# Kernel tuning notes

Hardware: AMD Instinct MI355X
Metric: run time of the kernel (lower is better)

The kernel has to match this reference:

```python
import jax, jax.numpy as jnp
import numpy as np

N_HEADS = 16
B, T, H, HA = 4, 8192, 1024, 1024

def _split_heads(x, n_heads):
    n, t, d = x.shape
    return x.reshape(n, t, n_heads, d // n_heads).transpose(0, 2, 1, 3)  # [n,h,t,dh]

def setup_inputs() -> dict:
    key = jax.random.key(0)
    ks = jax.random.split(key, 9)
    s = 0.02
    return {
        "q": jax.random.normal(ks[0], (B, T, H), jnp.float32),
        "k": jax.random.normal(ks[1], (B, T, H), jnp.float32),
        "v": jax.random.normal(ks[2], (B, T, H), jnp.float32),
        "mask_q": jnp.ones((B, T), jnp.float32),
        "mask_attn": jnp.ones((B, T), jnp.float32),
        "Wq": jax.random.normal(ks[3], (HA, H), jnp.float32) * s,
        "bq": jnp.zeros((HA,), jnp.float32),
        "Wk": jax.random.normal(ks[4], (HA, H), jnp.float32) * s,
        "bk": jnp.zeros((HA,), jnp.float32),
        "Wv": jax.random.normal(ks[5], (H, H), jnp.float32) * s,
        "bv": jnp.zeros((H,), jnp.float32),
    }

def reference(q, k, v, mask_q, mask_attn, Wq, bq, Wk, bk, Wv, bv):
    # projections (dropout = identity in eval)
    qp = q @ Wq.T + bq
    kp = k @ Wk.T + bk
    vp = v @ Wv.T + bv
    qh = _split_heads(qp, N_HEADS)  # [n,h,t,dqk]
    kh = _split_heads(kp, N_HEADS)
    vh = _split_heads(vp, N_HEADS)  # [n,h,t,dv]
    # additive masking (efficient_attn, outer_attn != 'scaled' branch)
    kh = kh - 10000.0 * (1.0 - mask_attn)[:, None, :, None]
    qh = qh - 10000.0 * (1.0 - mask_q)[:, None, :, None]
    dv = vh.shape[-1]  # d // n_heads where d = hidden (from v)
    # softmax over sequence dim of k, then k^T @ v : [n,h,dqk,dv]
    ctx = jnp.einsum('nhtd,nhte->nhde', jax.nn.softmax(kh, axis=2), vh)
    ctx = ctx / jnp.sqrt(jnp.float32(dv))
    # softmax over feature dim of q, then q @ ctx : [n,h,t,dv]
    out = jnp.einsum('nhtd,nhde->nhte', jax.nn.softmax(qh, axis=-1), ctx)
    n, h, t, e = out.shape
    return out.transpose(0, 2, 1, 3).reshape(n, t, h * e)
```

## Files before the change

### kernel.cpp

```cpp
#include <hip/hip_runtime.h>
#include <hip/hip_bf16.h>
#include <math.h>

#define B_  4
#define T_  8192
#define H_  1024
#define NHEAD 16
#define DH  64
#define BT  (B_*T_)

typedef __attribute__((ext_vector_type(8))) short bf16x8;
typedef __attribute__((ext_vector_type(4))) float f32x4;
typedef __attribute__((ext_vector_type(2))) float f32x2;
typedef __attribute__((ext_vector_type(2))) unsigned short u16x2;
typedef __attribute__((ext_vector_type(4))) unsigned short u16x4;
typedef __attribute__((ext_vector_type(8))) unsigned short u16x8;

static __device__ __forceinline__ float bf2f(unsigned short u) {
  union { unsigned int i; float f; } x; x.i = ((unsigned int)u) << 16; return x.f;
}
static __device__ __forceinline__ unsigned short f2bf(float f) {
  union { float f; unsigned int i; } x; x.f = f;
  unsigned int r = x.i + 0x7fffu + ((x.i >> 16) & 1u);
  return (unsigned short)(r >> 16);
}

#define GL2LDS(gptr, sptr) \
  __builtin_amdgcn_global_load_lds((const __attribute__((address_space(1))) void*)(gptr), \
                                   (__attribute__((address_space(3))) void*)(sptr), 16, 0, 0)

__global__ void cvt_kernel(const float* __restrict__ in, unsigned short* __restrict__ out, int n4) {
  int i = blockIdx.x * blockDim.x + threadIdx.x;
  int stride = gridDim.x * blockDim.x;
  for (int idx = i; idx < n4; idx += stride) {
    float4 v = reinterpret_cast<const float4*>(in)[idx];
    u16x4 o;
    o.x = f2bf(v.x); o.y = f2bf(v.y); o.z = f2bf(v.z); o.w = f2bf(v.w);
    reinterpret_cast<u16x4*>(out)[idx] = o;
  }
}

__global__ __launch_bounds__(256, 2) void gemm_nt(
    const unsigned short* __restrict__ A,
    const unsigned short* __restrict__ Bm,
    const float* __restrict__ bias,
    unsigned short* __restrict__ C) {
  const int K = 1024, N = 1024;
  __shared__ unsigned short sA[128 * 32];
  __shared__ unsigned short sB[128 * 32];
  const int tid  = threadIdx.x;
  const int lane = tid & 63;
  const int wid  = tid >> 6;
  const int orig = blockIdx.y * 8 + blockIdx.x;
  const int swz  = (orig & 7) * 256 + (orig >> 3);
  const int bm = (swz >> 3) * 128, bn = (swz & 7) * 128;
  const int wm = (wid >> 1) * 64,  wn = (wid & 1) * 64;

  f32x4 acc[4][4];
#pragma unroll
  for (int nn = 0; nn < 4; ++nn) {
    float bv = bias[bn + wn + nn * 16 + (lane & 15)];
    f32x4 sp = {bv, bv, bv, bv};
#pragma unroll
    for (int mm = 0; mm < 4; ++mm) acc[mm][nn] = sp;
  }

  const int srow = tid >> 2;
  const int scol = (tid & 3) * 8;
  const unsigned short* gA0 = A  + (size_t)(bm + srow) * K + scol;
  const unsigned short* gA1 = gA0 + (size_t)64 * K;
  const unsigned short* gB0 = Bm + (size_t)(bn + srow) * K + scol;
  const unsigned short* gB1 = gB0 + (size_t)64 * K;
  char* dA = (char*)&sA[0] + wid * 1024;
  char* dB = (char*)&sB[0] + wid * 1024;

  const char* fA = (const char*)&sA[0] + (wm + (lane & 15)) * 64 + (lane >> 4) * 16;
  const char* fB = (const char*)&sB[0] + (wn + (lane & 15)) * 64 + (lane >> 4) * 16;

  for (int k0 = 0; k0 < K; k0 += 32) {
    GL2LDS(gA0 + k0, dA);
    GL2LDS(gA1 + k0, dA + 4096);
    GL2LDS(gB0 + k0, dB);
    GL2LDS(gB1 + k0, dB + 4096);
    __syncthreads();
    bf16x8 av[4], bv_[4];
#pragma unroll
    for (int mm = 0; mm < 4; ++mm) av[mm]  = *(const bf16x8*)(fA + mm * 1024);
#pragma unroll
    for (int nn = 0; nn < 4; ++nn) bv_[nn] = *(const bf16x8*)(fB + nn * 1024);
#pragma unroll
    for (int mm = 0; mm < 4; ++mm)
#pragma unroll
      for (int nn = 0; nn < 4; ++nn)
        acc[mm][nn] = __builtin_amdgcn_mfma_f32_16x16x32_bf16(av[mm], bv_[nn], acc[mm][nn], 0, 0, 0);
    __syncthreads();
  }

  const int crow = bm + wm + (lane >> 4) * 4;
  const int ccol = bn + wn + (lane & 15);
#pragma unroll
  for (int mm = 0; mm < 4; ++mm)
#pragma unroll
    for (int j = 0; j < 4; ++j) {
      unsigned short* cp = C + (size_t)(crow + mm * 16 + j) * N + ccol;
#pragma unroll
      for (int nn = 0; nn < 4; ++nn) cp[nn * 16] = f2bf(acc[mm][nn][j]);
    }
}

__global__ __launch_bounds__(256, 2) void phase1(
    const unsigned short* __restrict__ Pk,
    const unsigned short* __restrict__ Pv,
    const float* __restrict__ mask_attn,
    float* __restrict__ Upart,
    float* __restrict__ cspart) {
  const int chunk = blockIdx.x;
  const int nh = blockIdx.y;
  const int n = nh >> 4, h = nh & 15;
  const int tid = threadIdx.x, lane = tid & 63, wid = tid >> 6;
  __shared__ __align__(16) unsigned short ekT[64 * 256];
  __shared__ __align__(16) unsigned short vpT[64 * 256];

  f32x4 acc[5];
#pragma unroll
  for (int i = 0; i < 5; ++i) acc[i] = (f32x4){0.f, 0.f, 0.f, 0.f};
  bf16x8 ones;
#pragma unroll
  for (int j = 0; j < 8; ++j) ones[j] = (short)0x3f80;

  const int isV = tid >> 7;
  const int slot0 = tid & 127;
  const unsigned short* src = isV ? Pv : Pk;
  unsigned short* dstT = isV ? vpT : ekT;

  const int arow = wid * 16 + (lane & 15);
  const int aswz = ((arow & 7) ^ ((arow >> 3) & 7)) << 4;

  for (int stage = 0; stage < 4; ++stage) {
    if (stage) __syncthreads();
#pragma unroll
    for (int r = 0; r < 2; ++r) {
      const int slot = slot0 + r * 128;
      const int toct = slot >> 3;
      const int d0   = (slot & 7) * 8;
      const int tbase = chunk * 1024 + stage * 256 + toct * 8;
      u16x8 in[8];
#pragma unroll
      for (int s = 0; s < 8; ++s)
        in[s] = *(const u16x8*)(src + (size_t)(n * T_ + tbase + s) * H_ + h * DH + d0);
      if (!isV) {
#pragma unroll
        for (int s = 0; s < 8; ++s) {
          const float madd = -10000.f * (1.f - mask_attn[n * T_ + tbase + s]);
          u16x8 o;
#pragma unroll
          for (int j = 0; j < 8; ++j) o[j] = f2bf(__expf(bf2f(in[s][j]) + madd));
          in[s] = o;
        }
      }
#pragma unroll
      for (int i = 0; i < 8; ++i) {
        u16x8 o;
#pragma unroll
        for (int s = 0; s < 8; ++s) o[s] = in[s][i];
        const int d = d0 + i;
        const int boff = (toct * 16) ^ (((d & 7) ^ ((d >> 3) & 7)) << 4);
        *(u16x8*)((char*)dstT + d * 512 + boff) = o;
      }
    }
    __syncthreads();
#pragma unroll
    for (int kk = 0; kk < 8; ++kk) {
      const int koff = kk * 64 + (lane >> 4) * 16;
      bf16x8 af = *(const bf16x8*)((const char*)ekT + arow * 512 + (koff ^ aswz));
      acc[4] = __builtin_amdgcn_mfma_f32_16x16x32_bf16(af, ones, acc[4], 0, 0, 0);
#pragma unroll
      for (int nn = 0; nn < 4; ++nn) {
        const int brow = nn * 16 + (lane & 15);
        const int bswz = ((brow & 7) ^ ((brow >> 3) & 7)) << 4;
        bf16x8 bf_ = *(const bf16x8*)((const char*)vpT + brow * 512 + (koff ^ bswz));
        acc[nn] = __builtin_amdgcn_mfma_f32_16x16x32_bf16(af, bf_, acc[nn], 0, 0, 0);
      }
    }
  }

  const int d = wid * 16 + (lane >> 4) * 4;
  const int e = lane & 15;
  float* up = Upart + ((size_t)(chunk * 64 + nh) * 64) * 64;
#pragma unroll
  for (int nn = 0; nn < 4; ++nn)
#pragma unroll
    for (int j = 0; j < 4; ++j)
      up[(size_t)(d + j) * 64 + nn * 16 + e] = acc[nn][j];
  if (e == 0)
#pragma unroll
    for (int j = 0; j < 4; ++j)
      cspart[((size_t)chunk * 64 + nh) * 64 + d + j] = acc[4][j];
}

__global__ void ctxbuild(const float* __restrict__ Upart,
                         const float* __restrict__ cspart,
                         unsigned short* __restrict__ ctxT) {
  const int nh = blockIdx.x, tid = threadIdx.x;
  __shared__ float cs[64];
  if (tid < 64) {
    float s = 0;
    for (int c = 0; c < 8; ++c) s += cspart[((size_t)c * 64 + nh) * 64 + tid];
    cs[tid] = s;
  }
  __syncthreads();
  const int d0 = (tid >> 4) * 4, e0 = (tid & 15) * 4;
#pragma unroll
  for (int i = 0; i < 4; ++i) {
    const float inv = 0.125f / cs[d0 + i];
#pragma unroll
    for (int j = 0; j < 4; ++j) {
      float s = 0;
      for (int c = 0; c < 8; ++c)
        s += Upart[((size_t)(c * 64 + nh) * 64 + d0 + i) * 64 + e0 + j];
      ctxT[((size_t)nh * 64 + (e0 + j)) * 64 + (d0 + i)] = f2bf(s * inv);
    }
  }
}

__global__ __launch_bounds__(256) void outk(
    const unsigned short* __restrict__ Pq,
    const unsigned short* __restrict__ ctxT,
    float* __restrict__ Out) {
  const int tb = blockIdx.x;
  const int nh = blockIdx.y;
  const int n = nh >> 4, h = nh & 15;
  const int tid = threadIdx.x, lane = tid & 63, wid = tid >> 6;
  __shared__ unsigned short sp[128][72];

  bf16x8 breg[2][4];
#pragma unroll
  for (int ks = 0; ks < 2; ++ks)
#pragma unroll
    for (int nn = 0; nn < 4; ++nn)
      breg[ks][nn] = *(const bf16x8*)(ctxT + ((size_t)nh * 64 + nn * 16 + (lane & 15)) * 64
                                      + ks * 32 + (lane >> 4) * 8);

  const int r = tid >> 1, half = tid & 1;
  const int t0 = tb * 128;
  const size_t qoff = (size_t)(n * T_ + t0 + r) * H_ + h * DH + half * 32;
  u16x8 qv[4];
#pragma unroll
  for (int s = 0; s < 4; ++s) qv[s] = *(const u16x8*)(Pq + qoff + s * 8);
  float e[32]; float sum = 0.f;
#pragma unroll
  for (int s = 0; s < 4; ++s)
#pragma unroll
    for (int j = 0; j < 8; ++j) { float x = __expf(bf2f(qv[s][j])); e[s * 8 + j] = x; sum += x; }
  sum += __shfl_xor(sum, 1);
  const float inv = 1.f / sum;
#pragma unroll
  for (int s = 0; s < 4; ++s) {
    u16x8 pb;
#pragma unroll
    for (int j = 0; j < 8; ++j) pb[j] = f2bf(e[s * 8 + j] * inv);
    *(u16x8*)&sp[r][half * 32 + s * 8] = pb;
  }
  __syncthreads();

  f32x4 acc[2][4];
  f32x4 z = {0.f, 0.f, 0.f, 0.f};
#pragma unroll
  for (int mm = 0; mm < 2; ++mm)
#pragma unroll
    for (int nn = 0; nn < 4; ++nn) acc[mm][nn] = z;
  const int wm = wid * 32;
#pragma unroll
  for (int ks = 0; ks < 2; ++ks) {
    bf16x8 av[2];
#pragma unroll
    for (int mm = 0; mm < 2; ++mm)
      av[mm] = *(const bf16x8*)((const char*)&sp[0][0]
               + (wm + mm * 16 + (lane & 15)) * 144 + ks * 64 + (lane >> 4) * 16);
#pragma unroll
    for (int mm = 0; mm < 2; ++mm)
#pragma unroll
      for (int nn = 0; nn < 4; ++nn)
        acc[mm][nn] = __builtin_amdgcn_mfma_f32_16x16x32_bf16(av[mm], breg[ks][nn], acc[mm][nn], 0, 0, 0);
  }

#pragma unroll
  for (int mm = 0; mm < 2; ++mm)
#pragma unroll
    for (int j = 0; j < 4; ++j) {
      const int row = t0 + wm + mm * 16 + (lane >> 4) * 4 + j;
      float* op = Out + ((size_t)n * T_ + row) * H_ + h * DH + (lane & 15);
#pragma unroll
      for (int nn = 0; nn < 4; ++nn) op[nn * 16] = acc[mm][nn][j];
    }
}

extern "C" void kernel_launch(void* const* d_in, const int* in_sizes, int n_in,
                              void* d_out, int out_size, void* d_ws, size_t ws_size,
                              hipStream_t stream) {
  const float* q  = (const float*)d_in[0];
  const float* k  = (const float*)d_in[1];
  const float* v  = (const float*)d_in[2];
  const float* mask_attn = (const float*)d_in[4];
  const float* Wq = (const float*)d_in[5];
  const float* bq = (const float*)d_in[6];
  const float* Wk = (const float*)d_in[7];
  const float* bk = (const float*)d_in[8];
  const float* Wv = (const float*)d_in[9];
  const float* bv = (const float*)d_in[10];
  float* out = (float*)d_out;

  char* ws = (char*)d_ws;
  size_t off = 0;
  unsigned short* Xb = (unsigned short*)(ws + off); off += (size_t)BT * H_ * 2;
  unsigned short* Wb = (unsigned short*)(ws + off); off += (size_t)3 * H_ * H_ * 2;
  unsigned short* Pq = (unsigned short*)(ws + off); off += (size_t)BT * H_ * 2;
  unsigned short* Pk = (unsigned short*)(ws + off); off += (size_t)BT * H_ * 2;
  unsigned short* Pv = (unsigned short*)(ws + off); off += (size_t)BT * H_ * 2;
  float* Upart  = (float*)(ws + off); off += (size_t)8 * 64 * 64 * 64 * 4;
  float* cspart = (float*)(ws + off); off += (size_t)8 * 64 * 64 * 4;
  unsigned short* ctxT = (unsigned short*)(ws + off); off += (size_t)64 * 64 * 64 * 2;

  dim3 blk(256);
  const int nW4 = H_ * H_ / 4;
  cvt_kernel<<<dim3(512), blk, 0, stream>>>(Wq, Wb + 0 * H_ * H_, nW4);
  cvt_kernel<<<dim3(512), blk, 0, stream>>>(Wk, Wb + 1 * H_ * H_, nW4);
  cvt_kernel<<<dim3(512), blk, 0, stream>>>(Wv, Wb + 2 * H_ * H_, nW4);

  const int nX4 = BT * H_ / 4;
  dim3 ggrid(8, 256);
  cvt_kernel<<<dim3(2048), blk, 0, stream>>>(k, Xb, nX4);
  gemm_nt<<<ggrid, blk, 0, stream>>>(Xb, Wb + 1 * H_ * H_, bk, Pk);
  cvt_kernel<<<dim3(2048), blk, 0, stream>>>(v, Xb, nX4);
  gemm_nt<<<ggrid, blk, 0, stream>>>(Xb, Wb + 2 * H_ * H_, bv, Pv);
  cvt_kernel<<<dim3(2048), blk, 0, stream>>>(q, Xb, nX4);
  gemm_nt<<<ggrid, blk, 0, stream>>>(Xb, Wb + 0 * H_ * H_, bq, Pq);

  phase1<<<dim3(8, 64), blk, 0, stream>>>(Pk, Pv, mask_attn, Upart, cspart);
  ctxbuild<<<dim3(64), blk, 0, stream>>>(Upart, cspart, ctxT);
  outk<<<dim3(64, 64), blk, 0, stream>>>(Pq, ctxT, out);
}
```

Before: 447.0 us.

## Replace projection GEMM with 256x256 double-buffered pipelined MFMA kernel

Rewrites the bf16 projection GEMM to use 256x256 block tiles with 8 waves, a 64-wide K step and two LDS buffers filled by direct global-to-LDS loads. A swizzled LDS layout reduces bank conflicts, and prefetching of the next tiles is interleaved with MFMA quadrants using raw barriers, manual vmcnt waits and priority hints. The aim is to raise arithmetic intensity and hide global-load latency that the old single-buffered 128x128 kernel exposed. It uses 128KB of LDS per block, which limits occupancy, and depends on hand-counted waitcnt correctness.

```diff
diff --git a/kernel.cpp b/kernel.cpp
--- a/kernel.cpp
+++ b/kernel.cpp
@@ -28,6 +28,9 @@
 #define GL2LDS(gptr, sptr) \
   __builtin_amdgcn_global_load_lds((const __attribute__((address_space(1))) void*)(gptr), \
                                    (__attribute__((address_space(3))) void*)(sptr), 16, 0, 0)
+
+#define BAR() do { asm volatile("" ::: "memory"); __builtin_amdgcn_s_barrier(); \
+                   asm volatile("" ::: "memory"); } while (0)
 
 __global__ void cvt_kernel(const float* __restrict__ in, unsigned short* __restrict__ out, int n4) {
   int i = blockIdx.x * blockDim.x + threadIdx.x;
@@ -40,71 +43,122 @@
   }
 }
 
-__global__ __launch_bounds__(256, 2) void gemm_nt(
+__global__ __launch_bounds__(512, 2) void gemm256(
     const unsigned short* __restrict__ A,
     const unsigned short* __restrict__ Bm,
     const float* __restrict__ bias,
     unsigned short* __restrict__ C) {
   const int K = 1024, N = 1024;
-  __shared__ unsigned short sA[128 * 32];
-  __shared__ unsigned short sB[128 * 32];
-  const int tid  = threadIdx.x;
-  const int lane = tid & 63;
-  const int wid  = tid >> 6;
-  const int orig = blockIdx.y * 8 + blockIdx.x;
-  const int swz  = (orig & 7) * 256 + (orig >> 3);
-  const int bm = (swz >> 3) * 128, bn = (swz & 7) * 128;
-  const int wm = (wid >> 1) * 64,  wn = (wid & 1) * 64;
-
-  f32x4 acc[4][4];
-#pragma unroll
-  for (int nn = 0; nn < 4; ++nn) {
-    float bv = bias[bn + wn + nn * 16 + (lane & 15)];
+  __shared__ char lds[131072];
+  const int tid = threadIdx.x, lane = tid & 63, wid = tid >> 6;
+  const int orig = blockIdx.x;
+  const int swzb = (orig & 7) * 64 + (orig >> 3);
+  const int bm = (swzb >> 2) * 256, bn = (swzb & 3) * 256;
+  const int wm = wid >> 2, wn = wid & 3;
+
+  const int sr   = wid * 8 + (lane >> 3);
+  const int scol = ((lane & 7) * 8) ^ ((lane & 32) >> 1);
+  const unsigned short* gA = A  + (size_t)(bm + sr) * K + scol;
+  const unsigned short* gB = Bm + (size_t)(bn + sr) * K + scol;
+  const int dstw = wid * 1024;
+
+  const int aflag = (lane & 4) ? 32 : 0;
+  const int lcol  = ((lane >> 4) * 16) ^ aflag;
+  const int aoff0 = (wm * 128 + (lane & 15)) * 128 + lcol;
+  const int boff0 = 32768 + (wn * 64 + (lane & 15)) * 128 + lcol;
+
+  f32x4 acc[8][4];
+#pragma unroll
+  for (int fn = 0; fn < 4; ++fn) {
+    float bv = bias[bn + wn * 64 + fn * 16 + (lane & 15)];
     f32x4 sp = {bv, bv, bv, bv};
 #pragma unroll
-    for (int mm = 0; mm < 4; ++mm) acc[mm][nn] = sp;
-  }
-
-  const int srow = tid >> 2;
-  const int scol = (tid & 3) * 8;
-  const unsigned short* gA0 = A  + (size_t)(bm + srow) * K + scol;
-  const unsigned short* gA1 = gA0 + (size_t)64 * K;
-  const unsigned short* gB0 = Bm + (size_t)(bn + srow) * K + scol;
-  const unsigned short* gB1 = gB0 + (size_t)64 * K;
-  char* dA = (char*)&sA[0] + wid * 1024;
-  char* dB = (char*)&sB[0] + wid * 1024;
-
-  const char* fA = (const char*)&sA[0] + (wm + (lane & 15)) * 64 + (lane >> 4) * 16;
-  const char* fB = (const char*)&sB[0] + (wn + (lane & 15)) * 64 + (lane >> 4) * 16;
-
-  for (int k0 = 0; k0 < K; k0 += 32) {
-    GL2LDS(gA0 + k0, dA);
-    GL2LDS(gA1 + k0, dA + 4096);
-    GL2LDS(gB0 + k0, dB);
-    GL2LDS(gB1 + k0, dB + 4096);
-    __syncthreads();
-    bf16x8 av[4], bv_[4];
-#pragma unroll
-    for (int mm = 0; mm < 4; ++mm) av[mm]  = *(const bf16x8*)(fA + mm * 1024);
-#pragma unroll
-    for (int nn = 0; nn < 4; ++nn) bv_[nn] = *(const bf16x8*)(fB + nn * 1024);
-#pragma unroll
-    for (int mm = 0; mm < 4; ++mm)
-#pragma unroll
-      for (int nn = 0; nn < 4; ++nn)
-        acc[mm][nn] = __builtin_amdgcn_mfma_f32_16x16x32_bf16(av[mm], bv_[nn], acc[mm][nn], 0, 0, 0);
-    __syncthreads();
-  }
-
-  const int crow = bm + wm + (lane >> 4) * 4;
-  const int ccol = bn + wn + (lane & 15);
-#pragma unroll
-  for (int mm = 0; mm < 4; ++mm)
+    for (int fm = 0; fm < 8; ++fm) acc[fm][fn] = sp;
+  }
+
+  bf16x8 aF[4][2], bF[4][2];
+
+  auto stA4 = [&](int buf, int kt) {
+    char* d = lds + buf * 65536 + dstw;
+    const unsigned short* g = gA + kt * 64;
+    GL2LDS(g, d);
+    GL2LDS(g + (size_t)64  * K, d + 8192);
+    GL2LDS(g + (size_t)128 * K, d + 16384);
+    GL2LDS(g + (size_t)192 * K, d + 24576);
+  };
+  auto stB = [&](int buf, int kt) {
+    char* d = lds + buf * 65536 + 32768 + dstw;
+    const unsigned short* g = gB + kt * 64;
+    GL2LDS(g, d);
+    GL2LDS(g + (size_t)64  * K, d + 8192);
+    GL2LDS(g + (size_t)128 * K, d + 16384);
+    GL2LDS(g + (size_t)192 * K, d + 24576);
+  };
+  auto loadA = [&](int buf, int mh) {
+#pragma unroll
+    for (int f = 0; f < 4; ++f)
+#pragma unroll
+      for (int ks = 0; ks < 2; ++ks)
+        aF[f][ks] = *(const bf16x8*)(lds + buf * 65536 + aoff0 + (mh * 4 + f) * 2048 + ks * 64);
+  };
+  auto loadB = [&](int buf, int nh) {
+#pragma unroll
+    for (int f = 0; f < 2; ++f)
+#pragma unroll
+      for (int ks = 0; ks < 2; ++ks)
+        bF[nh * 2 + f][ks] = *(const bf16x8*)(lds + buf * 65536 + boff0 + (nh * 2 + f) * 2048 + ks * 64);
+  };
+  auto quad = [&](int mh, int nh) {
+    __builtin_amdgcn_s_setprio(1);
+#pragma unroll
+    for (int f = 0; f < 4; ++f)
+#pragma unroll
+      for (int g2 = 0; g2 < 2; ++g2)
+#pragma unroll
+        for (int ks = 0; ks < 2; ++ks)
+          acc[mh * 4 + f][nh * 2 + g2] = __builtin_amdgcn_mfma_f32_16x16x32_bf16(
+              aF[f][ks], bF[nh * 2 + g2][ks], acc[mh * 4 + f][nh * 2 + g2], 0, 0, 0);
+    __builtin_amdgcn_s_setprio(0);
+  };
+
+  stA4(0, 0); stB(0, 0);
+  stA4(1, 1); stB(1, 1);
+  asm volatile("s_waitcnt vmcnt(8)" ::: "memory");
+  BAR();
+
+#define KTILE(t, STG, WSTR, DOW)                              \
+  {                                                           \
+    const int b_ = (t) & 1;                                   \
+    loadA(b_, 0); loadB(b_, 0);                               \
+    quad(0, 0);                                               \
+    BAR();                                                    \
+    loadB(b_, 1);                                             \
+    quad(0, 1);                                               \
+    BAR();                                                    \
+    if (STG) stB(b_, (t) + 2);                                \
+    loadA(b_, 1);                                             \
+    quad(1, 0);                                               \
+    BAR();                                                    \
+    if (STG) stA4(b_, (t) + 2);                               \
+    quad(1, 1);                                               \
+    if (DOW) { asm volatile("s_waitcnt vmcnt(" WSTR ")" ::: "memory"); } \
+    BAR();                                                    \
+  }
+
+  for (int t = 0; t < 14; ++t) KTILE(t, 1, "8", 1)
+  KTILE(14, 0, "0", 1)
+  KTILE(15, 0, "0", 0)
+#undef KTILE
+
+  const int crow0 = bm + wm * 128 + (lane >> 4) * 4;
+  const int ccol0 = bn + wn * 64 + (lane & 15);
+#pragma unroll
+  for (int fm = 0; fm < 8; ++fm)
 #pragma unroll
     for (int j = 0; j < 4; ++j) {
-      unsigned short* cp = C + (size_t)(crow + mm * 16 + j) * N + ccol;
-#pragma unroll
-      for (int nn = 0; nn < 4; ++nn) cp[nn * 16] = f2bf(acc[mm][nn][j]);
+      unsigned short* cp = C + (size_t)(crow0 + fm * 16 + j) * N + ccol0;
+#pragma unroll
+      for (int fn = 0; fn < 4; ++fn) cp[fn * 16] = f2bf(acc[fm][fn][j]);
     }
 }
 
@@ -328,13 +382,14 @@
   cvt_kernel<<<dim3(512), blk, 0, stream>>>(Wv, Wb + 2 * H_ * H_, nW4);
 
   const int nX4 = BT * H_ / 4;
-  dim3 ggrid(8, 256);
+  dim3 gblk(512);
+  dim3 ggrid(512);
   cvt_kernel<<<dim3(2048), blk, 0, stream>>>(k, Xb, nX4);
-  gemm_nt<<<ggrid, blk, 0, stream>>>(Xb, Wb + 1 * H_ * H_, bk, Pk);
+  gemm256<<<ggrid, gblk, 0, stream>>>(Xb, Wb + 1 * H_ * H_, bk, Pk);
   cvt_kernel<<<dim3(2048), blk, 0, stream>>>(v, Xb, nX4);
-  gemm_nt<<<ggrid, blk, 0, stream>>>(Xb, Wb + 2 * H_ * H_, bv, Pv);
+  gemm256<<<ggrid, gblk, 0, stream>>>(Xb, Wb + 2 * H_ * H_, bv, Pv);
   cvt_kernel<<<dim3(2048), blk, 0, stream>>>(q, Xb, nX4);
-  gemm_nt<<<ggrid, blk, 0, stream>>>(Xb, Wb + 0 * H_ * H_, bq, Pq);
+  gemm256<<<ggrid, gblk, 0, stream>>>(Xb, Wb + 0 * H_ * H_, bq, Pq);
 
   phase1<<<dim3(8, 64), blk, 0, stream>>>(Pk, Pv, mask_attn, Upart, cspart);
   ctxbuild<<<dim3(64), blk, 0, stream>>>(Upart, cspart, ctxT);
```

Measured after the change: 417.8 us. 6.5% less time.

## Fuse fp32-to-bf16 input conversion into double-buffered pipelined projection GEMM

Applied to the files above, without the earlier changes.

The separate activation conversion kernels are removed, and the projection GEMM now reads fp32 inputs directly. It converts them to bf16 in registers and writes them into swizzled LDS. The K loop is restructured into a double-buffered, software-pipelined schedule with manual waitcnt and barriers, plus s_setprio around the MFMAs. This removes three full read/write passes over the activations and aims to overlap global loads with MFMA. In exchange the GEMM reads the A operand from global memory at twice the bytes, and the hand-tuned waitcnt sequence is fragile.

```diff
diff --git a/kernel.cpp b/kernel.cpp
--- a/kernel.cpp
+++ b/kernel.cpp
@@ -28,6 +28,9 @@
 #define GL2LDS(gptr, sptr) \
   __builtin_amdgcn_global_load_lds((const __attribute__((address_space(1))) void*)(gptr), \
                                    (__attribute__((address_space(3))) void*)(sptr), 16, 0, 0)
+
+#define BAR() do { asm volatile("" ::: "memory"); __builtin_amdgcn_s_barrier(); \
+                   asm volatile("" ::: "memory"); } while (0)
 
 __global__ void cvt_kernel(const float* __restrict__ in, unsigned short* __restrict__ out, int n4) {
   int i = blockIdx.x * blockDim.x + threadIdx.x;
@@ -40,21 +43,32 @@
   }
 }
 
-__global__ __launch_bounds__(256, 2) void gemm_nt(
-    const unsigned short* __restrict__ A,
+__global__ __launch_bounds__(256, 3) void gemm128f(
+    const float* __restrict__ A,
     const unsigned short* __restrict__ Bm,
     const float* __restrict__ bias,
     unsigned short* __restrict__ C) {
   const int K = 1024, N = 1024;
-  __shared__ unsigned short sA[128 * 32];
-  __shared__ unsigned short sB[128 * 32];
-  const int tid  = threadIdx.x;
-  const int lane = tid & 63;
-  const int wid  = tid >> 6;
+  __shared__ char lds[32768];
+  const int tid = threadIdx.x, lane = tid & 63, wid = tid >> 6;
   const int orig = blockIdx.y * 8 + blockIdx.x;
   const int swz  = (orig & 7) * 256 + (orig >> 3);
   const int bm = (swz >> 3) * 128, bn = (swz & 7) * 128;
-  const int wm = (wid >> 1) * 64,  wn = (wid & 1) * 64;
+  const int wm = (wid >> 1) * 64, wn = (wid & 1) * 64;
+
+  const int r_  = tid >> 1;
+  const int ch  = (tid & 1) * 16;
+  const float* gA32 = A + (size_t)(bm + r_) * K + ch;
+  const int awbase = r_ * 64;
+  const int awswz  = ((r_ >> 1) & 3) << 4;
+
+  const int sr2  = wid * 16 + (lane >> 2);
+  const int scol = ((lane & 3) * 8) ^ (((lane >> 3) & 3) << 3);
+  const unsigned short* gB = Bm + (size_t)(bn + sr2) * K + scol;
+  const int dstw = wid * 1024;
+
+  const int fswz = (((lane & 15) >> 1) & 3) << 4;
+  const int kc   = ((lane >> 4) * 16) ^ fswz;
 
   f32x4 acc[4][4];
 #pragma unroll
@@ -65,36 +79,84 @@
     for (int mm = 0; mm < 4; ++mm) acc[mm][nn] = sp;
   }
 
-  const int srow = tid >> 2;
-  const int scol = (tid & 3) * 8;
-  const unsigned short* gA0 = A  + (size_t)(bm + srow) * K + scol;
-  const unsigned short* gA1 = gA0 + (size_t)64 * K;
-  const unsigned short* gB0 = Bm + (size_t)(bn + srow) * K + scol;
-  const unsigned short* gB1 = gB0 + (size_t)64 * K;
-  char* dA = (char*)&sA[0] + wid * 1024;
-  char* dB = (char*)&sB[0] + wid * 1024;
-
-  const char* fA = (const char*)&sA[0] + (wm + (lane & 15)) * 64 + (lane >> 4) * 16;
-  const char* fB = (const char*)&sB[0] + (wn + (lane & 15)) * 64 + (lane >> 4) * 16;
-
-  for (int k0 = 0; k0 < K; k0 += 32) {
-    GL2LDS(gA0 + k0, dA);
-    GL2LDS(gA1 + k0, dA + 4096);
-    GL2LDS(gB0 + k0, dB);
-    GL2LDS(gB1 + k0, dB + 4096);
-    __syncthreads();
-    bf16x8 av[4], bv_[4];
-#pragma unroll
-    for (int mm = 0; mm < 4; ++mm) av[mm]  = *(const bf16x8*)(fA + mm * 1024);
-#pragma unroll
-    for (int nn = 0; nn < 4; ++nn) bv_[nn] = *(const bf16x8*)(fB + nn * 1024);
+  f32x4 ar[4];
+  bf16x8 aF[4], bF[4];
+
+  auto issueA32 = [&](int kt) {
+    const float* g = gA32 + kt * 32;
+#pragma unroll
+    for (int j = 0; j < 4; ++j) ar[j] = *(const f32x4*)(g + j * 4);
+  };
+  auto writeA = [&](int buf) {
+#pragma unroll
+    for (int h = 0; h < 2; ++h) {
+      u16x8 o;
+#pragma unroll
+      for (int j = 0; j < 4; ++j) {
+        o[j]     = f2bf(ar[2 * h][j]);
+        o[4 + j] = f2bf(ar[2 * h + 1][j]);
+      }
+      *(u16x8*)(lds + buf * 16384 + awbase + ((ch * 2 + h * 16) ^ awswz)) = o;
+    }
+  };
+  auto stB = [&](int buf, int kt) {
+    char* d = lds + buf * 16384 + 8192 + dstw;
+    const unsigned short* g = gB + kt * 32;
+    GL2LDS(g, d);
+    GL2LDS(g + (size_t)64 * K, d + 4096);
+  };
+  auto loadFrags = [&](int buf) {
+#pragma unroll
+    for (int f = 0; f < 4; ++f)
+      aF[f] = *(const bf16x8*)(lds + buf * 16384 + (wm + f * 16 + (lane & 15)) * 64 + kc);
+#pragma unroll
+    for (int f = 0; f < 4; ++f)
+      bF[f] = *(const bf16x8*)(lds + buf * 16384 + 8192 + (wn + f * 16 + (lane & 15)) * 64 + kc);
+  };
+  auto mfma16 = [&]() {
+    __builtin_amdgcn_s_setprio(1);
 #pragma unroll
     for (int mm = 0; mm < 4; ++mm)
 #pragma unroll
       for (int nn = 0; nn < 4; ++nn)
-        acc[mm][nn] = __builtin_amdgcn_mfma_f32_16x16x32_bf16(av[mm], bv_[nn], acc[mm][nn], 0, 0, 0);
-    __syncthreads();
-  }
+        acc[mm][nn] = __builtin_amdgcn_mfma_f32_16x16x32_bf16(aF[mm], bF[nn], acc[mm][nn], 0, 0, 0);
+    __builtin_amdgcn_s_setprio(0);
+  };
+
+  issueA32(0);
+  asm volatile("s_waitcnt vmcnt(0)" ::: "memory");
+  writeA(0);
+  issueA32(1);
+  stB(0, 0); stB(1, 1);
+  asm volatile("s_waitcnt vmcnt(4)" ::: "memory");
+  writeA(1);
+  issueA32(2);
+  asm volatile("s_waitcnt vmcnt(6)" ::: "memory");
+  asm volatile("s_waitcnt lgkmcnt(0)" ::: "memory");
+  BAR();
+
+#define KBODY(t, STB_, DOW, WSTR, DOWRITE, DOISSUE)           \
+  {                                                           \
+    const int b_ = (t) & 1;                                   \
+    loadFrags(b_);                                            \
+    mfma16();                                                 \
+    BAR();                                                    \
+    if (STB_) stB(b_, (t) + 2);                               \
+    if (DOW) { asm volatile("s_waitcnt vmcnt(" WSTR ")" ::: "memory"); } \
+    if (DOWRITE) writeA(b_);                                  \
+    if (DOISSUE) issueA32((t) + 3);                           \
+    asm volatile("s_waitcnt lgkmcnt(0)" ::: "memory");        \
+    BAR();                                                    \
+  }
+
+  for (int t = 0; t < 29; ++t) KBODY(t, 1, 1, "2", 1, 1)
+  KBODY(29, 1, 1, "2", 1, 0)
+  KBODY(30, 0, 1, "0", 0, 0)
+  {
+    loadFrags(1);
+    mfma16();
+  }
+#undef KBODY
 
   const int crow = bm + wm + (lane >> 4) * 4;
   const int ccol = bn + wn + (lane & 15);
@@ -312,7 +374,6 @@
 
   char* ws = (char*)d_ws;
   size_t off = 0;
-  unsigned short* Xb = (unsigned short*)(ws + off); off += (size_t)BT * H_ * 2;
   unsigned short* Wb = (unsigned short*)(ws + off); off += (size_t)3 * H_ * H_ * 2;
   unsigned short* Pq = (unsigned short*)(ws + off); off += (size_t)BT * H_ * 2;
   unsigned short* Pk = (unsigned short*)(ws + off); off += (size_t)BT * H_ * 2;
@@ -327,14 +388,10 @@
   cvt_kernel<<<dim3(512), blk, 0, stream>>>(Wk, Wb + 1 * H_ * H_, nW4);
   cvt_kernel<<<dim3(512), blk, 0, stream>>>(Wv, Wb + 2 * H_ * H_, nW4);
 
-  const int nX4 = BT * H_ / 4;
   dim3 ggrid(8, 256);
-  cvt_kernel<<<dim3(2048), blk, 0, stream>>>(k, Xb, nX4);
-  gemm_nt<<<ggrid, blk, 0, stream>>>(Xb, Wb + 1 * H_ * H_, bk, Pk);
-  cvt_kernel<<<dim3(2048), blk, 0, stream>>>(v, Xb, nX4);
-  gemm_nt<<<ggrid, blk, 0, stream>>>(Xb, Wb + 2 * H_ * H_, bv, Pv);
-  cvt_kernel<<<dim3(2048), blk, 0, stream>>>(q, Xb, nX4);
-  gemm_nt<<<ggrid, blk, 0, stream>>>(Xb, Wb + 0 * H_ * H_, bq, Pq);
+  gemm128f<<<ggrid, blk, 0, stream>>>(k, Wb + 1 * H_ * H_, bk, Pk);
+  gemm128f<<<ggrid, blk, 0, stream>>>(v, Wb + 2 * H_ * H_, bv, Pv);
+  gemm128f<<<ggrid, blk, 0, stream>>>(q, Wb + 0 * H_ * H_, bq, Pq);
 
   phase1<<<dim3(8, 64), blk, 0, stream>>>(Pk, Pv, mask_attn, Upart, cspart);
   ctxbuild<<<dim3(64), blk, 0, stream>>>(Upart, cspart, ctxT);
```

After: 502.2 us. 1.12x slower.

## Double-buffer projection GEMM with K=64 tiles and swizzled LDS

Applied to the files above, without the earlier changes.

Rewrites the projection GEMM to stage 64-wide K tiles into two LDS buffers, prefetching two tiles ahead with direct global-to-LDS loads and partial vmcnt waits so loads overlap the MFMA work. It XOR-swizzles the LDS column layout to avoid bank conflicts on fragment reads and raises wave priority around the MFMA block. This removes the load-then-compute serialization and the two full syncthreads per 32-wide K step. In exchange LDS use grows to 64KB per block, which may limit occupancy to two blocks per CU.

```diff
diff --git a/kernel.cpp b/kernel.cpp
--- a/kernel.cpp
+++ b/kernel.cpp
@@ -28,6 +28,9 @@
 #define GL2LDS(gptr, sptr) \
   __builtin_amdgcn_global_load_lds((const __attribute__((address_space(1))) void*)(gptr), \
                                    (__attribute__((address_space(3))) void*)(sptr), 16, 0, 0)
+
+#define BAR() do { asm volatile("" ::: "memory"); __builtin_amdgcn_s_barrier(); \
+                   asm volatile("" ::: "memory"); } while (0)
 
 __global__ void cvt_kernel(const float* __restrict__ in, unsigned short* __restrict__ out, int n4) {
   int i = blockIdx.x * blockDim.x + threadIdx.x;
@@ -40,21 +43,28 @@
   }
 }
 
-__global__ __launch_bounds__(256, 2) void gemm_nt(
+__global__ __launch_bounds__(256, 2) void gemm128(
     const unsigned short* __restrict__ A,
     const unsigned short* __restrict__ Bm,
     const float* __restrict__ bias,
     unsigned short* __restrict__ C) {
   const int K = 1024, N = 1024;
-  __shared__ unsigned short sA[128 * 32];
-  __shared__ unsigned short sB[128 * 32];
-  const int tid  = threadIdx.x;
-  const int lane = tid & 63;
-  const int wid  = tid >> 6;
+  __shared__ char lds[65536];
+  const int tid = threadIdx.x, lane = tid & 63, wid = tid >> 6;
   const int orig = blockIdx.y * 8 + blockIdx.x;
   const int swz  = (orig & 7) * 256 + (orig >> 3);
   const int bm = (swz >> 3) * 128, bn = (swz & 7) * 128;
-  const int wm = (wid >> 1) * 64,  wn = (wid & 1) * 64;
+  const int wm = (wid >> 1) * 64, wn = (wid & 1) * 64;
+
+  const int sr   = wid * 8 + (lane >> 3);
+  const int scol = ((lane & 7) * 8) ^ ((lane >> 3) << 3);
+  const unsigned short* gA = A  + (size_t)(bm + sr) * K + scol;
+  const unsigned short* gB = Bm + (size_t)(bn + sr) * K + scol;
+  const int dstw = wid * 1024;
+
+  const int aswz = (lane & 7) << 4;
+  const int arow0 = (wm + (lane & 15)) * 128;
+  const int brow0 = 16384 + (wn + (lane & 15)) * 128;
 
   f32x4 acc[4][4];
 #pragma unroll
@@ -65,36 +75,68 @@
     for (int mm = 0; mm < 4; ++mm) acc[mm][nn] = sp;
   }
 
-  const int srow = tid >> 2;
-  const int scol = (tid & 3) * 8;
-  const unsigned short* gA0 = A  + (size_t)(bm + srow) * K + scol;
-  const unsigned short* gA1 = gA0 + (size_t)64 * K;
-  const unsigned short* gB0 = Bm + (size_t)(bn + srow) * K + scol;
-  const unsigned short* gB1 = gB0 + (size_t)64 * K;
-  char* dA = (char*)&sA[0] + wid * 1024;
-  char* dB = (char*)&sB[0] + wid * 1024;
-
-  const char* fA = (const char*)&sA[0] + (wm + (lane & 15)) * 64 + (lane >> 4) * 16;
-  const char* fB = (const char*)&sB[0] + (wn + (lane & 15)) * 64 + (lane >> 4) * 16;
-
-  for (int k0 = 0; k0 < K; k0 += 32) {
-    GL2LDS(gA0 + k0, dA);
-    GL2LDS(gA1 + k0, dA + 4096);
-    GL2LDS(gB0 + k0, dB);
-    GL2LDS(gB1 + k0, dB + 4096);
-    __syncthreads();
-    bf16x8 av[4], bv_[4];
-#pragma unroll
-    for (int mm = 0; mm < 4; ++mm) av[mm]  = *(const bf16x8*)(fA + mm * 1024);
-#pragma unroll
-    for (int nn = 0; nn < 4; ++nn) bv_[nn] = *(const bf16x8*)(fB + nn * 1024);
+  bf16x8 aF[4][2], bF[4][2];
+
+  auto stA = [&](int buf, int kt) {
+    char* d = lds + buf * 32768 + dstw;
+    const unsigned short* g = gA + kt * 64;
+#pragma unroll
+    for (int gg = 0; gg < 4; ++gg)
+      GL2LDS(g + (size_t)(gg * 32) * K, d + gg * 4096);
+  };
+  auto stB = [&](int buf, int kt) {
+    char* d = lds + buf * 32768 + 16384 + dstw;
+    const unsigned short* g = gB + kt * 64;
+#pragma unroll
+    for (int gg = 0; gg < 4; ++gg)
+      GL2LDS(g + (size_t)(gg * 32) * K, d + gg * 4096);
+  };
+  auto loadFrags = [&](int buf) {
+#pragma unroll
+    for (int f = 0; f < 4; ++f)
+#pragma unroll
+      for (int ks = 0; ks < 2; ++ks) {
+        const int col = (((lane >> 4) * 16 + ks * 64) ^ aswz);
+        aF[f][ks] = *(const bf16x8*)(lds + buf * 32768 + arow0 + f * 2048 + col);
+        bF[f][ks] = *(const bf16x8*)(lds + buf * 32768 + brow0 + f * 2048 + col);
+      }
+  };
+  auto mfma32 = [&]() {
+    __builtin_amdgcn_s_setprio(1);
 #pragma unroll
     for (int mm = 0; mm < 4; ++mm)
 #pragma unroll
       for (int nn = 0; nn < 4; ++nn)
-        acc[mm][nn] = __builtin_amdgcn_mfma_f32_16x16x32_bf16(av[mm], bv_[nn], acc[mm][nn], 0, 0, 0);
-    __syncthreads();
-  }
+#pragma unroll
+        for (int ks = 0; ks < 2; ++ks)
+          acc[mm][nn] = __builtin_amdgcn_mfma_f32_16x16x32_bf16(
+              aF[mm][ks], bF[nn][ks], acc[mm][nn], 0, 0, 0);
+    __builtin_amdgcn_s_setprio(0);
+  };
+
+  stA(0, 0); stB(0, 0);
+  stA(1, 1); stB(1, 1);
+  asm volatile("s_waitcnt vmcnt(8)" ::: "memory");
+  BAR();
+
+#define KT(t, STG, DOW, WSTR)                                 \
+  {                                                           \
+    const int b_ = (t) & 1;                                   \
+    loadFrags(b_);                                            \
+    mfma32();                                                 \
+    BAR();                                                    \
+    if (STG) { stA(b_, (t) + 2); stB(b_, (t) + 2); }          \
+    if (DOW) { asm volatile("s_waitcnt vmcnt(" WSTR ")" ::: "memory"); } \
+    BAR();                                                    \
+  }
+
+  for (int t = 0; t < 14; ++t) KT(t, 1, 1, "8")
+  KT(14, 0, 1, "0")
+  {
+    loadFrags(1);
+    mfma32();
+  }
+#undef KT
 
   const int crow = bm + wm + (lane >> 4) * 4;
   const int ccol = bn + wn + (lane & 15);
@@ -330,11 +372,11 @@
   const int nX4 = BT * H_ / 4;
   dim3 ggrid(8, 256);
   cvt_kernel<<<dim3(2048), blk, 0, stream>>>(k, Xb, nX4);
-  gemm_nt<<<ggrid, blk, 0, stream>>>(Xb, Wb + 1 * H_ * H_, bk, Pk);
+  gemm128<<<ggrid, blk, 0, stream>>>(Xb, Wb + 1 * H_ * H_, bk, Pk);
   cvt_kernel<<<dim3(2048), blk, 0, stream>>>(v, Xb, nX4);
-  gemm_nt<<<ggrid, blk, 0, stream>>>(Xb, Wb + 2 * H_ * H_, bv, Pv);
+  gemm128<<<ggrid, blk, 0, stream>>>(Xb, Wb + 2 * H_ * H_, bv, Pv);
   cvt_kernel<<<dim3(2048), blk, 0, stream>>>(q, Xb, nX4);
-  gemm_nt<<<ggrid, blk, 0, stream>>>(Xb, Wb + 0 * H_ * H_, bq, Pq);
+  gemm128<<<ggrid, blk, 0, stream>>>(Xb, Wb + 0 * H_ * H_, bq, Pq);
 
   phase1<<<dim3(8, 64), blk, 0, stream>>>(Pk, Pv, mask_attn, Upart, cspart);
   ctxbuild<<<dim3(64), blk, 0, stream>>>(Upart, cspart, ctxT);
```

After: 410.6 us. 1.09x faster.
